# Kernel tuning notes

Measured on AMD Instinct MI355X. Metric: run time of the kernel, lower is better.

Reference implementation:

```python
import jax, jax.numpy as jnp
import numpy as np

HIDDEN = 2048
N_EXPERTS = 8
N_LAYERS = 1
GATING_DIM = 64
TOP_K = 2
BALANCING_COEF = 0.01
NOISE_STD = 0.01
B = 4096


def setup_inputs() -> dict:
    key = jax.random.key(0)
    ks = jax.random.split(key, 12)
    s = 0.02
    return {
        "x": jax.random.normal(ks[0], (B, HIDDEN), jnp.float32),
        "noise": jax.random.normal(ks[1], (B, N_EXPERTS), jnp.float32),
        "gate_w1": jax.random.normal(ks[2], (HIDDEN, GATING_DIM), jnp.float32) * s,
        "gate_b1": jnp.zeros((GATING_DIM,), jnp.float32),
        "gate_w2": jax.random.normal(ks[3], (GATING_DIM, N_EXPERTS), jnp.float32) * s,
        "gate_b2": jnp.zeros((N_EXPERTS,), jnp.float32),
        "shared_w": jax.random.normal(ks[4], (HIDDEN, HIDDEN), jnp.float32) * s,
        "shared_b": jnp.zeros((HIDDEN,), jnp.float32),
        "shared_scale": jnp.float32(1.0),
        "expert_w": jax.random.normal(ks[5], (N_EXPERTS, N_LAYERS, HIDDEN, HIDDEN), jnp.float32) * s,
        "expert_b": jnp.zeros((N_EXPERTS, N_LAYERS, HIDDEN), jnp.float32),
        "router_scale": jnp.float32(1.0),
    }


def reference(x, noise, gate_w1, gate_b1, gate_w2, gate_b2,
              shared_w, shared_b, shared_scale, expert_w, expert_b, router_scale):
    Bn = x.shape[0]
    # gating network: softmax(Linear(ReLU(Linear(x)))) + noise
    h = jax.nn.relu(x @ gate_w1 + gate_b1)
    gating = jax.nn.softmax(h @ gate_w2 + gate_b2, axis=-1) + noise * NOISE_STD  # [B,E]

    topk_w, topk_idx = jax.lax.top_k(gating, TOP_K)  # [B,K]
    topk_w = topk_w / jnp.sum(topk_w, axis=-1, keepdims=True)

    # dense combine weights [B,E] (zero for unrouted experts)
    comb = jnp.zeros((Bn, N_EXPERTS), x.dtype)
    comb = comb.at[jnp.arange(Bn)[:, None], topk_idx].add(topk_w)

    # all experts on all tokens (same math as masked dispatch) -> [E,B,D]
    eh = jnp.broadcast_to(x[None], (N_EXPERTS, Bn, HIDDEN))
    for l in range(N_LAYERS):
        eh = jax.nn.sigmoid(jnp.einsum('ebd,edf->ebf', eh, expert_w[:, l]) + expert_b[:, l][:, None, :]) + eh
    routed = jnp.einsum('ebd,be->bd', eh, comb)

    shared = jax.nn.sigmoid(x @ shared_w + shared_b)
    final_out = x + shared_scale * shared + router_scale * routed

    experts_prob = jnp.mean(gating, axis=0)
    target_prob = jnp.ones((N_EXPERTS,), x.dtype) / N_EXPERTS
    gate_loss = jnp.mean((target_prob - experts_prob) ** 2) * BALANCING_COEF
    return final_out, gate_loss
```

## Files before the change

### kernel.cpp

```cpp
#include <hip/hip_runtime.h>
#include <cstdint>
#include <cstddef>

#define HIDDEN 2048
#define NEXP 8
#define GDIM 64
#define BTOK 4096
#define NOISE_STD 0.01f

#define BM 128
#define BN 128
#define BK 32
#define NT_K (HIDDEN / BK)

typedef unsigned short ushort_t;
typedef short bf16x8 __attribute__((ext_vector_type(8)));
typedef float f32x4 __attribute__((ext_vector_type(4)));
typedef unsigned short ushortx8 __attribute__((ext_vector_type(8)));

__device__ __forceinline__ float sigmoid_fast(float v) {
    return 1.0f / (1.0f + __expf(-v));
}

__device__ __forceinline__ ushort_t f2bf(float f) {
    union { float f; uint32_t u; } v; v.f = f;
    uint32_t r = v.u + 0x7fffu + ((v.u >> 16) & 1u);
    return (ushort_t)(r >> 16);
}

__device__ __forceinline__ void gl2lds16(const ushort_t* g, ushort_t* l) {
    __builtin_amdgcn_global_load_lds(
        (const __attribute__((address_space(1))) unsigned int*)g,
        (__attribute__((address_space(3))) unsigned int*)l, 16, 0, 0);
}

__global__ __launch_bounds__(256) void convert_x_kernel(
    const float* __restrict__ in, ushort_t* __restrict__ out)
{
    const size_t i = ((size_t)blockIdx.x * 256 + threadIdx.x) * 8;
    float4 a = *(const float4*)(in + i);
    float4 b = *(const float4*)(in + i + 4);
    ushortx8 o;
    o[0] = f2bf(a.x); o[1] = f2bf(a.y); o[2] = f2bf(a.z); o[3] = f2bf(a.w);
    o[4] = f2bf(b.x); o[5] = f2bf(b.y); o[6] = f2bf(b.z); o[7] = f2bf(b.w);
    *(ushortx8*)(out + i) = o;
}

__global__ __launch_bounds__(256) void transpose_convert_kernel(
    const float* __restrict__ in, ushort_t* __restrict__ out)
{
    __shared__ float t[64][65];
    const size_t moff = (size_t)blockIdx.z * HIDDEN * HIDDEN;
    const int r0 = blockIdx.y * 64, c0 = blockIdx.x * 64;
    const int tid = threadIdx.x;
    const int tr = tid >> 4, tc = (tid & 15) * 4;
    #pragma unroll
    for (int ii = 0; ii < 4; ++ii) {
        float4 v = *(const float4*)(in + moff + (size_t)(r0 + tr + ii * 16) * HIDDEN + c0 + tc);
        t[tr + ii * 16][tc + 0] = v.x; t[tr + ii * 16][tc + 1] = v.y;
        t[tr + ii * 16][tc + 2] = v.z; t[tr + ii * 16][tc + 3] = v.w;
    }
    __syncthreads();
    const int orow = tid >> 3;
    const int ok = (tid & 7) * 8;
    #pragma unroll
    for (int jj = 0; jj < 2; ++jj) {
        const int c = orow + jj * 32;
        ushortx8 o;
        #pragma unroll
        for (int e = 0; e < 8; ++e) o[e] = f2bf(t[ok + e][c]);
        *(ushortx8*)(out + moff + (size_t)(c0 + c) * HIDDEN + r0 + ok) = o;
    }
}

__global__ __launch_bounds__(256) void gating_kernel(
    const float* __restrict__ x, const float* __restrict__ noise,
    const float* __restrict__ gw1, const float* __restrict__ gb1,
    const float* __restrict__ gw2, const float* __restrict__ gb2,
    float* __restrict__ gating_out, float* __restrict__ wlist,
    int* __restrict__ tlist, int* __restrict__ counts)
{
    const int token = blockIdx.x;
    const int tid = threadIdx.x;
    const int j = tid & 63;
    const int part = tid >> 6;

    __shared__ float hpart[4][GDIM];
    __shared__ float gate_s[NEXP];

    const float* xr = x + (size_t)token * HIDDEN;
    float s = 0.f;
    const int d0 = part * (HIDDEN / 4);
    #pragma unroll 4
    for (int d = d0; d < d0 + HIDDEN / 4; ++d)
        s = fmaf(xr[d], gw1[(size_t)d * GDIM + j], s);
    hpart[part][j] = s;
    __syncthreads();

    if (tid < GDIM) {
        float h = hpart[0][tid] + hpart[1][tid] + hpart[2][tid] + hpart[3][tid] + gb1[tid];
        hpart[0][tid] = fmaxf(h, 0.f);
    }
    __syncthreads();

    if (tid < NEXP) {
        float l = gb2[tid];
        #pragma unroll
        for (int jj = 0; jj < GDIM; ++jj)
            l = fmaf(hpart[0][jj], gw2[jj * NEXP + tid], l);
        gate_s[tid] = l;
    }
    __syncthreads();

    if (tid == 0) {
        float g[NEXP];
        float m = gate_s[0];
        #pragma unroll
        for (int e = 1; e < NEXP; ++e) m = fmaxf(m, gate_s[e]);
        float se = 0.f;
        #pragma unroll
        for (int e = 0; e < NEXP; ++e) { g[e] = expf(gate_s[e] - m); se += g[e]; }
        float inv = 1.0f / se;
        #pragma unroll
        for (int e = 0; e < NEXP; ++e) {
            g[e] = g[e] * inv + noise[(size_t)token * NEXP + e] * NOISE_STD;
            gating_out[(size_t)token * NEXP + e] = g[e];
        }
        int i1 = 0;
        #pragma unroll
        for (int e = 1; e < NEXP; ++e) if (g[e] > g[i1]) i1 = e;
        int i2 = (i1 == 0) ? 1 : 0;
        #pragma unroll
        for (int e = 0; e < NEXP; ++e) if (e != i1 && g[e] > g[i2]) i2 = e;
        float wsum = g[i1] + g[i2];
        int p1 = atomicAdd(&counts[i1], 1);
        tlist[i1 * BTOK + p1] = token; wlist[i1 * BTOK + p1] = g[i1] / wsum;
        int p2 = atomicAdd(&counts[i2], 1);
        tlist[i2 * BTOK + p2] = token; wlist[i2 * BTOK + p2] = g[i2] / wsum;
    }
}

__global__ __launch_bounds__(256) void loss_kernel(
    const float* __restrict__ gating, float* __restrict__ out_loss)
{
    __shared__ float red[256][NEXP];
    const int tid = threadIdx.x;
    float loc[NEXP];
    #pragma unroll
    for (int e = 0; e < NEXP; ++e) loc[e] = 0.f;
    for (int t = tid; t < BTOK; t += 256) {
        #pragma unroll
        for (int e = 0; e < NEXP; ++e) loc[e] += gating[(size_t)t * NEXP + e];
    }
    #pragma unroll
    for (int e = 0; e < NEXP; ++e) red[tid][e] = loc[e];
    __syncthreads();
    for (int s = 128; s > 0; s >>= 1) {
        if (tid < s) {
            #pragma unroll
            for (int e = 0; e < NEXP; ++e) red[tid][e] += red[tid + s][e];
        }
        __syncthreads();
    }
    if (tid == 0) {
        float loss = 0.f;
        #pragma unroll
        for (int e = 0; e < NEXP; ++e) {
            float p = red[0][e] / (float)BTOK;
            float d = 0.125f - p;
            loss += d * d;
        }
        out_loss[0] = (loss / 8.0f) * 0.01f;
    }
}

__global__ __launch_bounds__(256) void expert_kernel(
    const ushort_t* __restrict__ xb, const ushort_t* __restrict__ ewT,
    const float* __restrict__ eb, const int* __restrict__ counts,
    const int* __restrict__ tlist, const float* __restrict__ wlist,
    float* __restrict__ routed)
{
    const int e = blockIdx.z;
    const int cnt = counts[e];
    const int m0 = blockIdx.y * BM;
    if (m0 >= cnt) return;
    const int n0 = blockIdx.x * BN;
    const ushort_t* __restrict__ wT = ewT + (size_t)e * HIDDEN * HIDDEN;

    __shared__ int rows_s[BM];
    __shared__ float wts_s[BM];
    __shared__ ushort_t sA[2][BM * BK];
    __shared__ ushort_t sB[2][BN * BK];

    const int tid = threadIdx.x;
    if (tid < BM) {
        int mi = m0 + tid;
        if (mi < cnt) { rows_s[tid] = tlist[e * BTOK + mi]; wts_s[tid] = wlist[e * BTOK + mi]; }
        else { rows_s[tid] = -1; wts_s[tid] = 0.f; }
    }
    __syncthreads();

    const int lane = tid & 63;
    const int wid = tid >> 6;
    const int wr = (wid >> 1) * 64;
    const int wc = (wid & 1) * 64;
    const int lr = lane & 15;
    const int sg = (lane >> 4) ^ ((lane >> 1) & 3);

    const int crow = wid * 32 + (lane >> 2);
    const int kgr = (((lane & 3) ^ ((lane >> 3) & 3)) << 3);
    const int tokA0 = max(rows_s[crow], 0);
    const int tokA1 = max(rows_s[crow + 16], 0);
    const ushort_t* srcA0 = xb + (size_t)tokA0 * HIDDEN + kgr;
    const ushort_t* srcA1 = xb + (size_t)tokA1 * HIDDEN + kgr;
    const ushort_t* srcB0 = wT + (size_t)(n0 + crow) * HIDDEN + kgr;
    const ushort_t* srcB1 = wT + (size_t)(n0 + crow + 16) * HIDDEN + kgr;

    f32x4 acc[4][4];
    #pragma unroll
    for (int m = 0; m < 4; ++m)
        #pragma unroll
        for (int n = 0; n < 4; ++n) acc[m][n] = (f32x4){0.f, 0.f, 0.f, 0.f};

    gl2lds16(srcA0, &sA[0][(wid * 32) * BK]);
    gl2lds16(srcA1, &sA[0][(wid * 32 + 16) * BK]);
    gl2lds16(srcB0, &sB[0][(wid * 32) * BK]);
    gl2lds16(srcB1, &sB[0][(wid * 32 + 16) * BK]);
    __syncthreads();

    int cur = 0;
    for (int kt = 0; kt < NT_K; ++kt) {
        if (kt + 1 < NT_K) {
            const int k0 = (kt + 1) * BK;
            gl2lds16(srcA0 + k0, &sA[cur ^ 1][(wid * 32) * BK]);
            gl2lds16(srcA1 + k0, &sA[cur ^ 1][(wid * 32 + 16) * BK]);
            gl2lds16(srcB0 + k0, &sB[cur ^ 1][(wid * 32) * BK]);
            gl2lds16(srcB1 + k0, &sB[cur ^ 1][(wid * 32 + 16) * BK]);
        }
        const ushort_t* Ab = sA[cur];
        const ushort_t* Bb = sB[cur];
        bf16x8 af[4], bfr[4];
        #pragma unroll
        for (int m = 0; m < 4; ++m)
            af[m] = *(const bf16x8*)&Ab[(wr + m * 16 + lr) * BK + sg * 8];
        #pragma unroll
        for (int n = 0; n < 4; ++n)
            bfr[n] = *(const bf16x8*)&Bb[(wc + n * 16 + lr) * BK + sg * 8];
        #pragma unroll
        for (int m = 0; m < 4; ++m)
            #pragma unroll
            for (int n = 0; n < 4; ++n)
                acc[m][n] = __builtin_amdgcn_mfma_f32_16x16x32_bf16(af[m], bfr[n], acc[m][n], 0, 0, 0);
        __syncthreads();
        cur ^= 1;
    }

    float bvn[4];
    #pragma unroll
    for (int n = 0; n < 4; ++n)
        bvn[n] = eb[(size_t)e * HIDDEN + n0 + wc + n * 16 + lr];
    #pragma unroll
    for (int m = 0; m < 4; ++m) {
        #pragma unroll
        for (int q = 0; q < 4; ++q) {
            const int lrow = wr + m * 16 + (lane >> 4) * 4 + q;
            const int r = rows_s[lrow];
            if (r < 0) continue;
            const float wt = wts_s[lrow];
            float* dst = routed + (size_t)r * HIDDEN + n0 + wc + lr;
            #pragma unroll
            for (int n = 0; n < 4; ++n)
                atomicAdd(dst + n * 16, wt * sigmoid_fast(acc[m][n][q] + bvn[n]));
        }
    }
}

__global__ __launch_bounds__(256) void shared_final_kernel(
    const ushort_t* __restrict__ xb, const ushort_t* __restrict__ swT,
    const float* __restrict__ x, const float* __restrict__ bias,
    const float* __restrict__ sscale, const float* __restrict__ rscale,
    const float* __restrict__ routed, float* __restrict__ out)
{
    const int m0 = blockIdx.y * BM;
    const int n0 = blockIdx.x * BN;

    __shared__ ushort_t sA[2][BM * BK];
    __shared__ ushort_t sB[2][BN * BK];

    const int tid = threadIdx.x;
    const int lane = tid & 63;
    const int wid = tid >> 6;
    const int wr = (wid >> 1) * 64;
    const int wc = (wid & 1) * 64;
    const int lr = lane & 15;
    const int sg = (lane >> 4) ^ ((lane >> 1) & 3);

    const int crow = wid * 32 + (lane >> 2);
    const int kgr = (((lane & 3) ^ ((lane >> 3) & 3)) << 3);
    const ushort_t* srcA0 = xb + (size_t)(m0 + crow) * HIDDEN + kgr;
    const ushort_t* srcA1 = xb + (size_t)(m0 + crow + 16) * HIDDEN + kgr;
    const ushort_t* srcB0 = swT + (size_t)(n0 + crow) * HIDDEN + kgr;
    const ushort_t* srcB1 = swT + (size_t)(n0 + crow + 16) * HIDDEN + kgr;

    f32x4 acc[4][4];
    #pragma unroll
    for (int m = 0; m < 4; ++m)
        #pragma unroll
        for (int n = 0; n < 4; ++n) acc[m][n] = (f32x4){0.f, 0.f, 0.f, 0.f};

    gl2lds16(srcA0, &sA[0][(wid * 32) * BK]);
    gl2lds16(srcA1, &sA[0][(wid * 32 + 16) * BK]);
    gl2lds16(srcB0, &sB[0][(wid * 32) * BK]);
    gl2lds16(srcB1, &sB[0][(wid * 32 + 16) * BK]);
    __syncthreads();

    int cur = 0;
    for (int kt = 0; kt < NT_K; ++kt) {
        if (kt + 1 < NT_K) {
            const int k0 = (kt + 1) * BK;
            gl2lds16(srcA0 + k0, &sA[cur ^ 1][(wid * 32) * BK]);
            gl2lds16(srcA1 + k0, &sA[cur ^ 1][(wid * 32 + 16) * BK]);
            gl2lds16(srcB0 + k0, &sB[cur ^ 1][(wid * 32) * BK]);
            gl2lds16(srcB1 + k0, &sB[cur ^ 1][(wid * 32 + 16) * BK]);
        }
        const ushort_t* Ab = sA[cur];
        const ushort_t* Bb = sB[cur];
        bf16x8 af[4], bfr[4];
        #pragma unroll
        for (int m = 0; m < 4; ++m)
            af[m] = *(const bf16x8*)&Ab[(wr + m * 16 + lr) * BK + sg * 8];
        #pragma unroll
        for (int n = 0; n < 4; ++n)
            bfr[n] = *(const bf16x8*)&Bb[(wc + n * 16 + lr) * BK + sg * 8];
        #pragma unroll
        for (int m = 0; m < 4; ++m)
            #pragma unroll
            for (int n = 0; n < 4; ++n)
                acc[m][n] = __builtin_amdgcn_mfma_f32_16x16x32_bf16(af[m], bfr[n], acc[m][n], 0, 0, 0);
        __syncthreads();
        cur ^= 1;
    }

    const float ss = *sscale;
    const float rs = *rscale;
    float bvn[4];
    #pragma unroll
    for (int n = 0; n < 4; ++n)
        bvn[n] = bias[n0 + wc + n * 16 + lr];
    #pragma unroll
    for (int m = 0; m < 4; ++m) {
        #pragma unroll
        for (int q = 0; q < 4; ++q) {
            const int row = m0 + wr + m * 16 + (lane >> 4) * 4 + q;
            const size_t base = (size_t)row * HIDDEN + n0 + wc + lr;
            #pragma unroll
            for (int n = 0; n < 4; ++n) {
                const float xv = x[base + n * 16];
                const float rv = routed[base + n * 16];
                out[base + n * 16] = xv + ss * sigmoid_fast(acc[m][n][q] + bvn[n]) + rs * (xv + rv);
            }
        }
    }
}

extern "C" void kernel_launch(void* const* d_in, const int* in_sizes, int n_in,
                              void* d_out, int out_size, void* d_ws, size_t ws_size,
                              hipStream_t stream) {
    const float* x      = (const float*)d_in[0];
    const float* noise  = (const float*)d_in[1];
    const float* gw1    = (const float*)d_in[2];
    const float* gb1    = (const float*)d_in[3];
    const float* gw2    = (const float*)d_in[4];
    const float* gb2    = (const float*)d_in[5];
    const float* sw     = (const float*)d_in[6];
    const float* sb     = (const float*)d_in[7];
    const float* sscale = (const float*)d_in[8];
    const float* ew     = (const float*)d_in[9];
    const float* ebias  = (const float*)d_in[10];
    const float* rscale = (const float*)d_in[11];
    float* out = (float*)d_out;

    float* ws = (float*)d_ws;
    float* routed   = ws;
    int*   counts   = (int*)(ws + (size_t)BTOK * HIDDEN);
    float* gating   = ws + (size_t)BTOK * HIDDEN + 8;
    int*   tlist    = (int*)(gating + (size_t)BTOK * NEXP);
    float* wlist    = (float*)(tlist + (size_t)NEXP * BTOK);
    ushort_t* xb    = (ushort_t*)(wlist + (size_t)NEXP * BTOK);
    ushort_t* ewT   = xb + (size_t)BTOK * HIDDEN;
    ushort_t* swT   = ewT + (size_t)NEXP * HIDDEN * HIDDEN;

    hipMemsetAsync(d_ws, 0, ((size_t)BTOK * HIDDEN + 8) * sizeof(float), stream);

    convert_x_kernel<<<(BTOK * HIDDEN) / (256 * 8), 256, 0, stream>>>(x, xb);
    transpose_convert_kernel<<<dim3(HIDDEN / 64, HIDDEN / 64, NEXP), 256, 0, stream>>>(ew, ewT);
    transpose_convert_kernel<<<dim3(HIDDEN / 64, HIDDEN / 64, 1), 256, 0, stream>>>(sw, swT);

    gating_kernel<<<BTOK, 256, 0, stream>>>(x, noise, gw1, gb1, gw2, gb2,
                                            gating, wlist, tlist, counts);
    loss_kernel<<<1, 256, 0, stream>>>(gating, out + (size_t)BTOK * HIDDEN);

    expert_kernel<<<dim3(HIDDEN / BN, BTOK / BM, NEXP), 256, 0, stream>>>(
        xb, ewT, ebias, counts, tlist, wlist, routed);
    shared_final_kernel<<<dim3(HIDDEN / BN, BTOK / BM), 256, 0, stream>>>(
        xb, swT, x, sb, sscale, rscale, routed, out);
}
```

Baseline: 757.6 us.

## Process eight tokens per gating block to reuse gate weight loads

New measurement: 727.4 us. 1.04x faster.

```diff
diff --git a/kernel.cpp b/kernel.cpp
--- a/kernel.cpp
+++ b/kernel.cpp
@@ -12,6 +12,7 @@
 #define BN 128
 #define BK 32
 #define NT_K (HIDDEN / BK)
+#define GTOK 8
 
 typedef unsigned short ushort_t;
 typedef short bf16x8 __attribute__((ext_vector_type(8)));
@@ -80,46 +81,56 @@
     float* __restrict__ gating_out, float* __restrict__ wlist,
     int* __restrict__ tlist, int* __restrict__ counts)
 {
-    const int token = blockIdx.x;
     const int tid = threadIdx.x;
-    const int j = tid & 63;
-    const int part = tid >> 6;
-
-    __shared__ float hpart[4][GDIM];
-    __shared__ float gate_s[NEXP];
-
-    const float* xr = x + (size_t)token * HIDDEN;
-    float s = 0.f;
-    const int d0 = part * (HIDDEN / 4);
-    #pragma unroll 4
-    for (int d = d0; d < d0 + HIDDEN / 4; ++d)
-        s = fmaf(xr[d], gw1[(size_t)d * GDIM + j], s);
-    hpart[part][j] = s;
-    __syncthreads();
-
-    if (tid < GDIM) {
-        float h = hpart[0][tid] + hpart[1][tid] + hpart[2][tid] + hpart[3][tid] + gb1[tid];
-        hpart[0][tid] = fmaxf(h, 0.f);
-    }
-    __syncthreads();
-
-    if (tid < NEXP) {
-        float l = gb2[tid];
-        #pragma unroll
-        for (int jj = 0; jj < GDIM; ++jj)
-            l = fmaf(hpart[0][jj], gw2[jj * NEXP + tid], l);
-        gate_s[tid] = l;
-    }
-    __syncthreads();
-
-    if (tid == 0) {
+    const int t0 = blockIdx.x * GTOK;
+
+    __shared__ float xs[GTOK][64];
+    __shared__ float hs[GTOK][GDIM + 1];
+    __shared__ float logit_s[GTOK][NEXP];
+
+    const int tok = tid >> 5;
+    const int jj = (tid & 31) * 2;
+    float accx = 0.f, accy = 0.f;
+
+    for (int kc = 0; kc < HIDDEN / 64; ++kc) {
+        const int k0 = kc * 64;
+        __syncthreads();
+        if (tid < 128) {
+            const int r = tid >> 4, c4 = (tid & 15) * 4;
+            *(float4*)&xs[r][c4] = *(const float4*)(x + (size_t)(t0 + r) * HIDDEN + k0 + c4);
+        }
+        __syncthreads();
+        #pragma unroll 8
+        for (int kk = 0; kk < 64; ++kk) {
+            const float xv = xs[tok][kk];
+            const float2 g = *(const float2*)(gw1 + (size_t)(k0 + kk) * GDIM + jj);
+            accx = fmaf(xv, g.x, accx);
+            accy = fmaf(xv, g.y, accy);
+        }
+    }
+    hs[tok][jj]     = fmaxf(accx + gb1[jj], 0.f);
+    hs[tok][jj + 1] = fmaxf(accy + gb1[jj + 1], 0.f);
+    __syncthreads();
+
+    if (tid < GTOK * NEXP) {
+        const int t = tid >> 3, e = tid & 7;
+        float l = gb2[e];
+        #pragma unroll
+        for (int j2 = 0; j2 < GDIM; ++j2)
+            l = fmaf(hs[t][j2], gw2[j2 * NEXP + e], l);
+        logit_s[t][e] = l;
+    }
+    __syncthreads();
+
+    if (tid < GTOK) {
+        const int token = t0 + tid;
         float g[NEXP];
-        float m = gate_s[0];
-        #pragma unroll
-        for (int e = 1; e < NEXP; ++e) m = fmaxf(m, gate_s[e]);
+        float m = logit_s[tid][0];
+        #pragma unroll
+        for (int e = 1; e < NEXP; ++e) m = fmaxf(m, logit_s[tid][e]);
         float se = 0.f;
         #pragma unroll
-        for (int e = 0; e < NEXP; ++e) { g[e] = expf(gate_s[e] - m); se += g[e]; }
+        for (int e = 0; e < NEXP; ++e) { g[e] = expf(logit_s[tid][e] - m); se += g[e]; }
         float inv = 1.0f / se;
         #pragma unroll
         for (int e = 0; e < NEXP; ++e) {
@@ -396,8 +407,8 @@
     transpose_convert_kernel<<<dim3(HIDDEN / 64, HIDDEN / 64, NEXP), 256, 0, stream>>>(ew, ewT);
     transpose_convert_kernel<<<dim3(HIDDEN / 64, HIDDEN / 64, 1), 256, 0, stream>>>(sw, swT);
 
-    gating_kernel<<<BTOK, 256, 0, stream>>>(x, noise, gw1, gb1, gw2, gb2,
-                                            gating, wlist, tlist, counts);
+    gating_kernel<<<BTOK / GTOK, 256, 0, stream>>>(x, noise, gw1, gb1, gw2, gb2,
+                                                   gating, wlist, tlist, counts);
     loss_kernel<<<1, 256, 0, stream>>>(gating, out + (size_t)BTOK * HIDDEN);
 
     expert_kernel<<<dim3(HIDDEN / BN, BTOK / BM, NEXP), 256, 0, stream>>>(
```
